# Performance work log

Measured on AMD Instinct MI355X. Metric: run time of the kernel, lower is better.

## Reference

```python
import jax, jax.numpy as jnp
import numpy as np
from jax import lax

B, T, I, H, ZH, NZ, L = 64, 512, 64, 512, 128, 32, 3


def setup_inputs() -> dict:
    key = jax.random.key(0)
    ks = jax.random.split(key, 20)
    s_h = 1.0 / np.sqrt(H)
    s_z = 1.0 / np.sqrt(ZH)
    rnd = lambda k, shape, s: jax.random.uniform(k, shape, jnp.float32, -s, s)
    return {
        "xs": jax.random.normal(ks[0], (B, T, I), jnp.float32),
        "cond": jax.random.normal(ks[1], (B, I), jnp.float32),
        "h_c": jnp.zeros((1, B, H), jnp.float32),
        "h_c_hat": jnp.zeros((1, B, ZH), jnp.float32),
        # hyper GRU (LearnableCell, num_layers=3 gates)
        "hyper_x2h_w": rnd(ks[2], (3 * ZH, I + H), s_z),
        "hyper_x2h_b": rnd(ks[3], (3 * ZH,), s_z),
        "hyper_h2h_w": rnd(ks[4], (3 * ZH, ZH), s_z),
        "hyper_h2h_b": rnd(ks[5], (3 * ZH,), s_z),
        # hypernet projections
        "zh_w": rnd(ks[6], (L * NZ, ZH), s_h),
        "zh_b": rnd(ks[7], (L * NZ,), s_h),
        "zx_w": rnd(ks[8], (L * NZ, ZH), s_h),
        "zx_b": rnd(ks[9], (L * NZ,), s_h),
        "zb_w": rnd(ks[10], (L * NZ, ZH), s_h),
        # per-layer embedding->scale projections
        "dh_w": rnd(ks[11], (L, H, NZ), s_h),
        "dx_w": rnd(ks[12], (L, H, NZ), s_h),
        "db_w": rnd(ks[13], (L, H, NZ), s_h),
        "db_b": rnd(ks[14], (L, H), s_h),
        # main recurrent / input weights
        "wh": jax.random.normal(ks[15], (L, H, H), jnp.float32) * s_h,
        "wx": jax.random.normal(ks[16], (L, H, I), jnp.float32) * s_h,
    }


def reference(xs, cond, h_c, h_c_hat,
              hyper_x2h_w, hyper_x2h_b, hyper_h2h_w, hyper_h2h_b,
              zh_w, zh_b, zx_w, zx_b, zb_w,
              dh_w, dx_w, db_w, db_b, wh, wx):
    nz = zh_w.shape[0] // 3

    def step(carry, x_t):  # x_t: [B, I]
        h, hhat = carry  # [B, H], [B, ZH]
        # --- hyper GRU update ---
        x_hat = jnp.concatenate([h, cond], axis=-1)  # [B, H+I]
        ih = x_hat @ hyper_x2h_w.T + hyper_x2h_b     # [B, 3*ZH]
        hh = hhat @ hyper_h2h_w.T + hyper_h2h_b
        i_r, i_i, i_n = jnp.split(ih, 3, axis=-1)
        h_r, h_i, h_n = jnp.split(hh, 3, axis=-1)
        r = jax.nn.sigmoid(i_r + h_r)
        g = jax.nn.sigmoid(i_i + h_i)
        n = jnp.tanh(i_n + r * h_n)
        hhat_new = n + g * (hhat - n)                # [B, ZH]
        # --- hypernetwork embeddings ---
        zh = (hhat_new @ zh_w.T + zh_b).reshape(-1, 3, nz)  # [B, 3, nz]
        zx = (hhat_new @ zx_w.T + zx_b).reshape(-1, 3, nz)
        zb = (hhat_new @ zb_w.T).reshape(-1, 3, nz)
        dh = jnp.einsum('blz,lhz->blh', zh, dh_w)    # [B, 3, H]
        dx = jnp.einsum('blz,lhz->blh', zx, dx_w)
        db = jnp.einsum('blz,lhz->blh', zb, db_w) + db_b
        # --- main GRU with hyper-modulated weights ---
        whh = jnp.einsum('bh,lgh->blg', h, wh)       # [B, 3, H]
        wxx = jnp.einsum('bi,lgi->blg', x_t, wx)
        pre = dh * whh + dx * wxx + db               # [B, 3, H]
        r0 = jax.nn.sigmoid(pre[:, 0])
        g0 = jax.nn.sigmoid(pre[:, 1])
        n0 = jnp.tanh(r0 * dh[:, 2] * whh[:, 2] + dx[:, 2] * wxx[:, 2] + db[:, 2])
        h_new = n0 + g0 * (h - n0)                   # [B, H]
        return (h_new, hhat_new), h_new

    xs_t = jnp.swapaxes(xs, 0, 1)  # [T, B, I]
    (h_f, hhat_f), ys = lax.scan(step, (h_c[0], h_c_hat[0]), xs_t)
    out = jnp.swapaxes(ys, 0, 1)   # [B, T, H]
    return out, h_f[None], hhat_f[:, None]  # final states: [1,B,H], [B,1,ZH]
```

## Files before the change

kernel.cpp:

```cpp
#include <hip/hip_runtime.h>
#include <math.h>

#define BB  64
#define TT  512
#define IN  64
#define HH  512
#define ZHH 128
#define NT  1024

#define OFF_EXIH   0u
#define OFF_EXH    196608u
#define OFF_FLAG   327680u
#define OFF_WH     335872u
#define OFF_WX     1908736u
#define OFF_DW     2105344u
#define OFF_X2H    2400256u
#define OFF_H2HB   2842624u
#define OFF_ZWB    2940928u
#define WS_NOX2H   2400256u
#define WS_FULL    2842624u
#define WS_XTRA    3014656u

__device__ __forceinline__ float sigmoidf_(float x) {
    return 1.0f / (1.0f + __expf(-x));
}
__device__ __forceinline__ float tanhf_(float x) {
    return 2.0f / (1.0f + __expf(-2.0f * x)) - 1.0f;
}
__device__ __forceinline__ float bflo(unsigned u) { return __uint_as_float(u << 16); }
__device__ __forceinline__ float bfhi(unsigned u) { return __uint_as_float(u & 0xffff0000u); }
__device__ __forceinline__ unsigned short f2bf(float f) {
    unsigned u = __float_as_uint(f);
    return (unsigned short)((u + 0x7fffu + ((u >> 16) & 1u)) >> 16);
}
__device__ __forceinline__ float dotbf8(uint4 U, float4 a, float4 b) {
    return bflo(U.x)*a.x + bfhi(U.x)*a.y + bflo(U.y)*a.z + bfhi(U.y)*a.w
         + bflo(U.z)*b.x + bfhi(U.z)*b.y + bflo(U.w)*b.z + bfhi(U.w)*b.w;
}
__device__ __forceinline__ float dot4_(const float4 a, const float4 b) {
    return a.x*b.x + a.y*b.y + a.z*b.z + a.w*b.w;
}
__device__ __forceinline__ uint4 packbf8(const float* s) {
    float4 a = *(const float4*)s;
    float4 c = *(const float4*)(s + 4);
    uint4 q;
    q.x = (unsigned)f2bf(a.x) | ((unsigned)f2bf(a.y) << 16);
    q.y = (unsigned)f2bf(a.z) | ((unsigned)f2bf(a.w) << 16);
    q.z = (unsigned)f2bf(c.x) | ((unsigned)f2bf(c.y) << 16);
    q.w = (unsigned)f2bf(c.z) | ((unsigned)f2bf(c.w) << 16);
    return q;
}

__global__ __launch_bounds__(256)
void pack_w(const float* __restrict__ wh, const float* __restrict__ wx,
            const float* __restrict__ dh_w, const float* __restrict__ dx_w,
            const float* __restrict__ db_w, const float* __restrict__ x2h_w,
            const float* __restrict__ h2h_w, const float* __restrict__ zh_w,
            const float* __restrict__ zx_w, const float* __restrict__ zb_w,
            int packX2H, int packHZ, char* __restrict__ wsb)
{
    const int u = blockIdx.x * 256 + threadIdx.x;
    if (u < 98304) {
        int q = u / 24576, r1 = u % 24576, k8 = r1 / 384, rr = r1 % 384;
        int g = rr >> 7, hl = rr & 127, h = q*128 + hl;
        ((uint4*)(wsb + OFF_WH))[u] = packbf8(wh + ((size_t)(g*512 + h))*512 + k8*8);
    } else if (u < 110592) {
        int v = u - 98304;
        int q = v / 3072, r1 = v % 3072, k8 = r1 / 384, rr = r1 % 384;
        int g = rr >> 7, hl = rr & 127, h = q*128 + hl;
        ((uint4*)(wsb + OFF_WX))[v] = packbf8(wx + ((size_t)(g*512 + h))*64 + k8*8);
    } else if (u < 129024) {
        int v = u - 110592;
        int q = v / 4608, r1 = v % 4608, k8 = r1 / 1152, rr = r1 % 1152;
        int u9 = rr >> 7, hl = rr & 127, h = q*128 + hl;
        int kind = u9 / 3, l = u9 - kind*3;
        const float* dsrc = (kind == 0) ? dh_w : ((kind == 1) ? dx_w : db_w);
        ((uint4*)(wsb + OFF_DW))[v] = packbf8(dsrc + ((size_t)(l*512) + h)*32 + k8*8);
    } else if (u < 156672) {
        if (!packX2H) return;
        int v = u - 129024;
        int q = v / 6912, r1 = v % 6912, k8 = r1 / 96, rr = r1 % 96;
        int g = rr >> 5, zz = rr & 31, j = g*128 + q*32 + zz;
        ((uint4*)(wsb + OFF_X2H))[v] = packbf8(x2h_w + (size_t)j*576 + k8*8);
    } else if (u < 162816) {
        if (!packHZ) return;
        int v = u - 156672;
        int q = v / 1536, r1 = v % 1536, k8 = r1 / 96, rr = r1 % 96;
        int g = rr >> 5, zz = rr & 31, j = g*128 + q*32 + zz;
        ((uint4*)(wsb + OFF_H2HB))[v] = packbf8(h2h_w + (size_t)j*128 + k8*8);
    } else if (u < 167424) {
        if (!packHZ) return;
        int v = u - 162816;
        int k8 = v / 288, r = v % 288;
        const float* src = (r < 96) ? (zh_w + (size_t)r*128)
                         : ((r < 192) ? (zx_w + (size_t)(r - 96)*128)
                                      : (zb_w + (size_t)(r - 192)*128));
        ((uint4*)(wsb + OFF_ZWB))[v] = packbf8(src + k8*8);
    }
}

template<int X2HP, int HZP>
__global__ __launch_bounds__(NT)
void hypercell_q(
    const float* __restrict__ xs, const float* __restrict__ cond,
    const float* __restrict__ h_c, const float* __restrict__ h_c_hat,
    const float* __restrict__ x2h_w, const float* __restrict__ x2h_b,
    const float* __restrict__ h2h_w, const float* __restrict__ h2h_b,
    const float* __restrict__ zh_w, const float* __restrict__ zh_b,
    const float* __restrict__ zx_w, const float* __restrict__ zx_b,
    const float* __restrict__ zb_w, const float* __restrict__ db_b,
    char* __restrict__ wsb, float* __restrict__ out)
{
    __shared__ __align__(16) float sh_h[512];
    __shared__ __align__(16) float sh_hat[128];
    __shared__ __align__(16) float sh_x[64];
    __shared__ __align__(16) float sh_c[64];
    __shared__ __align__(16) float sh_z[288];
    __shared__ float sh_whhp[768];
    __shared__ float sh_wxx[384];
    __shared__ float sh_ihp[192];
    __shared__ float sh_d[1152];
    __shared__ float sh_bih[96];
    __shared__ float sh_bhh[96];
    __shared__ float sh_bz[288];
    __shared__ float sh_bdb[384];

    const int b   = blockIdx.x & 63;
    const int q   = blockIdx.x >> 6;
    const int tid = threadIdx.x;

    const uint4* WHq   = (const uint4*)(wsb + OFF_WH)   + q*24576;
    const uint4* WXq   = (const uint4*)(wsb + OFF_WX)   + q*3072;
    const uint4* DWq   = (const uint4*)(wsb + OFF_DW)   + q*4608;
    const uint4* X2Hq  = (const uint4*)(wsb + OFF_X2H)  + q*6912;
    const uint4* H2HBq = (const uint4*)(wsb + OFF_H2HB) + q*1536;
    const uint4* ZWB   = (const uint4*)(wsb + OFF_ZWB);

    float* exch_ihhh = (float*)(wsb + OFF_EXIH) + (size_t)b*768;
    float* exch_h    = (float*)(wsb + OFF_EXH)  + (size_t)b*512;
    int* flagA = (int*)(wsb + OFF_FLAG + (size_t)b*64);
    int* flagB = (int*)(wsb + OFF_FLAG + 4096 + (size_t)b*64);

    if (tid < 96) {
        int j = (tid >> 5)*128 + q*32 + (tid & 31);
        sh_bih[tid] = x2h_b[j];
        sh_bhh[tid] = h2h_b[j];
    }
    if (tid < 288) sh_bz[tid] = (tid < 96) ? zh_b[tid]
                              : ((tid < 192) ? zx_b[tid - 96] : 0.f);
    if (tid < 384) {
        int l = tid >> 7, hl = tid & 127;
        sh_bdb[tid] = db_b[l*512 + q*128 + hl];
    }
    if (tid < 512) sh_h[tid] = h_c[(size_t)b*512 + tid];
    if (tid < 128) sh_hat[tid] = h_c_hat[(size_t)b*128 + tid];
    if (tid < 64) {
        sh_c[tid] = cond[(size_t)b*64 + tid];
        sh_x[tid] = xs[(size_t)b*TT*IN + tid];
    }
    __syncthreads();

    for (int t = 0; t < TT; ++t) {
        const float4* h4 = (const float4*)sh_h;
        if (tid < 768) {
            const int half = (tid >= 384);
            const int rr = half ? (tid - 384) : tid;
            const uint4* W0 = WHq + (half ? 32*384 : 0) + rr;
            const float4* hblk = h4 + half*64;
            float a0 = 0.f;
            #pragma unroll 8
            for (int k8 = 0; k8 < 32; ++k8)
                a0 += dotbf8(W0[k8*384], hblk[2*k8], hblk[2*k8 + 1]);
            sh_whhp[half*384 + rr] = a0;
            if (!half) {
                float a1 = 0.f;
                const uint4* X0 = WXq + rr;
                const float4* x4 = (const float4*)sh_x;
                #pragma unroll
                for (int k8 = 0; k8 < 8; ++k8)
                    a1 += dotbf8(X0[k8*384], x4[2*k8], x4[2*k8 + 1]);
                sh_wxx[rr] = a1;
            }
        } else if (tid < 960) {
            const int u = tid - 768;
            const int half = (u >= 96);
            const int rr = half ? (u - 96) : u;
            float a = half ? 0.f : sh_bih[rr];
            if (X2HP) {
                const uint4* W0 = X2Hq + rr;
                if (!half) {
                    #pragma unroll 4
                    for (int k8 = 0; k8 < 36; ++k8)
                        a += dotbf8(W0[k8*96], h4[2*k8], h4[2*k8 + 1]);
                } else {
                    #pragma unroll 4
                    for (int k8 = 36; k8 < 64; ++k8)
                        a += dotbf8(W0[k8*96], h4[2*k8], h4[2*k8 + 1]);
                    const float4* c4 = (const float4*)sh_c;
                    #pragma unroll
                    for (int k8 = 64; k8 < 72; ++k8)
                        a += dotbf8(W0[k8*96], c4[2*(k8-64)], c4[2*(k8-64) + 1]);
                }
            } else {
                const int j = (rr >> 5)*128 + q*32 + (rr & 31);
                const float4* wr = (const float4*)(x2h_w + (size_t)j*576);
                if (!half) {
                    #pragma unroll 8
                    for (int k4 = 0; k4 < 72; ++k4) a += dot4_(wr[k4], h4[k4]);
                } else {
                    #pragma unroll 8
                    for (int k4 = 72; k4 < 128; ++k4) a += dot4_(wr[k4], h4[k4]);
                    const float4* c4 = (const float4*)sh_c;
                    #pragma unroll
                    for (int k4 = 128; k4 < 144; ++k4) a += dot4_(wr[k4], c4[k4 - 128]);
                }
            }
            sh_ihp[half*96 + rr] = a;
        } else {
            const int t3 = tid - 960;
            const float4* hat4 = (const float4*)sh_hat;
            #pragma unroll
            for (int p = 0; p < 2; ++p) {
                const int rr = t3 + 64*p;
                if (rr < 96) {
                    const int j = (rr >> 5)*128 + q*32 + (rr & 31);
                    float a = sh_bhh[rr];
                    if (HZP) {
                        const uint4* W = H2HBq + rr;
                        #pragma unroll 8
                        for (int k8 = 0; k8 < 16; ++k8)
                            a += dotbf8(W[k8*96], hat4[2*k8], hat4[2*k8 + 1]);
                    } else {
                        const float4* wr = (const float4*)(h2h_w + (size_t)j*128);
                        #pragma unroll 8
                        for (int k4 = 0; k4 < 32; ++k4) a += dot4_(wr[k4], hat4[k4]);
                    }
                    __hip_atomic_store(&exch_ihhh[384 + j], a, __ATOMIC_RELAXED, __HIP_MEMORY_SCOPE_AGENT);
                }
            }
        }
        __syncthreads();
        if (tid < 96) {
            const int j = (tid >> 5)*128 + q*32 + (tid & 31);
            __hip_atomic_store(&exch_ihhh[j], sh_ihp[tid] + sh_ihp[96 + tid],
                               __ATOMIC_RELAXED, __HIP_MEMORY_SCOPE_AGENT);
        }
        asm volatile("s_waitcnt vmcnt(0)" ::: "memory");
        __syncthreads();
        if (tid == 0) {
            __hip_atomic_fetch_add(flagA, 1, __ATOMIC_RELAXED, __HIP_MEMORY_SCOPE_AGENT);
            while (__hip_atomic_load(flagA, __ATOMIC_RELAXED, __HIP_MEMORY_SCOPE_AGENT) < 4*(t+1))
                __builtin_amdgcn_s_sleep(1);
        }
        __syncthreads();

        if (tid < 128) {
            const int j = tid;
            float i_r = __hip_atomic_load(&exch_ihhh[j],       __ATOMIC_RELAXED, __HIP_MEMORY_SCOPE_AGENT);
            float i_i = __hip_atomic_load(&exch_ihhh[128 + j], __ATOMIC_RELAXED, __HIP_MEMORY_SCOPE_AGENT);
            float i_n = __hip_atomic_load(&exch_ihhh[256 + j], __ATOMIC_RELAXED, __HIP_MEMORY_SCOPE_AGENT);
            float h_r = __hip_atomic_load(&exch_ihhh[384 + j], __ATOMIC_RELAXED, __HIP_MEMORY_SCOPE_AGENT);
            float h_i = __hip_atomic_load(&exch_ihhh[512 + j], __ATOMIC_RELAXED, __HIP_MEMORY_SCOPE_AGENT);
            float h_n = __hip_atomic_load(&exch_ihhh[640 + j], __ATOMIC_RELAXED, __HIP_MEMORY_SCOPE_AGENT);
            float rg = sigmoidf_(i_r + h_r);
            float gg = sigmoidf_(i_i + h_i);
            float nn = tanhf_(i_n + rg * h_n);
            float hn = nn + gg * (sh_hat[j] - nn);
            sh_hat[j] = hn;
            if (t == TT - 1 && q == 0)
                __builtin_nontemporal_store(hn,
                    &out[(size_t)BB*TT*HH + (size_t)BB*HH + (size_t)b*ZHH + j]);
        } else if (tid >= 128 && tid < 192 && t + 1 < TT) {
            sh_x[tid - 128] = xs[((size_t)b*TT + t + 1)*IN + (tid - 128)];
        }
        __syncthreads();

        if (tid < 288) {
            float acc = sh_bz[tid];
            const float4* hat4 = (const float4*)sh_hat;
            if (HZP) {
                const uint4* W = ZWB + tid;
                #pragma unroll 8
                for (int k8 = 0; k8 < 16; ++k8)
                    acc += dotbf8(W[k8*288], hat4[2*k8], hat4[2*k8 + 1]);
            } else {
                const float* src = (tid < 96) ? (zh_w + (size_t)tid*128)
                                 : ((tid < 192) ? (zx_w + (size_t)(tid - 96)*128)
                                                : (zb_w + (size_t)(tid - 192)*128));
                const float4* W = (const float4*)src;
                #pragma unroll 8
                for (int k4 = 0; k4 < 32; ++k4) acc += dot4_(W[k4], hat4[k4]);
            }
            sh_z[tid] = acc;
        }
        __syncthreads();

        #pragma unroll
        for (int rp = 0; rp < 2; ++rp) {
            const int rr = tid + rp*NT;
            if (rr < 1152) {
                const int u9 = rr >> 7;
                const int kind = u9 / 3, l = u9 - kind*3;
                const uint4* W = DWq + rr;
                const float4* Z = (const float4*)(&sh_z[kind*96 + l*32]);
                float acc = 0.f;
                #pragma unroll
                for (int k8 = 0; k8 < 4; ++k8)
                    acc += dotbf8(W[k8*1152], Z[2*k8], Z[2*k8 + 1]);
                sh_d[rr] = acc;
            }
        }
        __syncthreads();

        if (tid < 128) {
            const int hl = tid, hg = q*128 + hl;
            float whh0 = sh_whhp[hl]       + sh_whhp[384 + hl];
            float whh1 = sh_whhp[128 + hl] + sh_whhp[512 + hl];
            float whh2 = sh_whhp[256 + hl] + sh_whhp[640 + hl];
            float wxx0 = sh_wxx[hl], wxx1 = sh_wxx[128 + hl], wxx2 = sh_wxx[256 + hl];
            float dh0 = sh_d[hl],       dh1 = sh_d[128 + hl], dh2 = sh_d[256 + hl];
            float dx0 = sh_d[384 + hl], dx1 = sh_d[512 + hl], dx2 = sh_d[640 + hl];
            float db0 = sh_d[768 + hl]  + sh_bdb[hl];
            float db1 = sh_d[896 + hl]  + sh_bdb[128 + hl];
            float db2 = sh_d[1024 + hl] + sh_bdb[256 + hl];
            float r0 = sigmoidf_(dh0*whh0 + dx0*wxx0 + db0);
            float g0 = sigmoidf_(dh1*whh1 + dx1*wxx1 + db1);
            float n0 = tanhf_(r0*dh2*whh2 + dx2*wxx2 + db2);
            float hold = sh_h[hg];
            float hnew = n0 + g0*(hold - n0);
            __builtin_nontemporal_store(hnew, &out[((size_t)b*TT + t)*HH + hg]);
            if (t == TT - 1)
                __builtin_nontemporal_store(hnew, &out[(size_t)BB*TT*HH + (size_t)b*512 + hg]);
            __hip_atomic_store(&exch_h[hg], hnew, __ATOMIC_RELAXED, __HIP_MEMORY_SCOPE_AGENT);
        }
        asm volatile("s_waitcnt vmcnt(0)" ::: "memory");
        __syncthreads();
        if (tid == 0) {
            __hip_atomic_fetch_add(flagB, 1, __ATOMIC_RELAXED, __HIP_MEMORY_SCOPE_AGENT);
            while (__hip_atomic_load(flagB, __ATOMIC_RELAXED, __HIP_MEMORY_SCOPE_AGENT) < 4*(t+1))
                __builtin_amdgcn_s_sleep(1);
        }
        __syncthreads();
        if (tid < 512)
            sh_h[tid] = __hip_atomic_load(&exch_h[tid], __ATOMIC_RELAXED, __HIP_MEMORY_SCOPE_AGENT);
        __syncthreads();
    }
}

__device__ __forceinline__ float wred(float v) {
    v += __shfl_xor(v, 32, 64); v += __shfl_xor(v, 16, 64); v += __shfl_xor(v, 8, 64);
    v += __shfl_xor(v, 4, 64);  v += __shfl_xor(v, 2, 64);  v += __shfl_xor(v, 1, 64);
    return v;
}
__global__ __launch_bounds__(1024)
void hypercell_batch(
    const float* __restrict__ xs, const float* __restrict__ cond,
    const float* __restrict__ h_c, const float* __restrict__ h_c_hat,
    const float* __restrict__ x2h_w, const float* __restrict__ x2h_b,
    const float* __restrict__ h2h_w, const float* __restrict__ h2h_b,
    const float* __restrict__ zh_w, const float* __restrict__ zh_b,
    const float* __restrict__ zx_w, const float* __restrict__ zx_b,
    const float* __restrict__ zb_w,
    const float* __restrict__ dh_w, const float* __restrict__ dx_w,
    const float* __restrict__ db_w, const float* __restrict__ db_b,
    const float* __restrict__ wh, const float* __restrict__ wx,
    float* __restrict__ out)
{
    __shared__ float h_s[HH];
    __shared__ float hhat_s[ZHH];
    __shared__ float x_s[IN];
    __shared__ float cond_s[IN];
    __shared__ float whh_s[3*HH];
    __shared__ float wxx_s[3*HH];
    __shared__ float ih_s[3*ZHH];
    __shared__ float hh_s[3*ZHH];
    __shared__ float z_s[288];
    const int b = blockIdx.x, tid = threadIdx.x, lane = tid & 63, wv = tid >> 6;
    if (tid < IN)  cond_s[tid] = cond[(size_t)b*IN + tid];
    if (tid < HH)  h_s[tid]    = h_c[(size_t)b*HH + tid];
    if (tid < ZHH) hhat_s[tid] = h_c_hat[(size_t)b*ZHH + tid];
    __syncthreads();
    for (int t = 0; t < TT; ++t) {
        if (tid < IN) x_s[tid] = xs[((size_t)b*TT + t)*IN + tid];
        const float4* h4 = (const float4*)h_s;
        const float4 ha = h4[lane]; const float4 hb = h4[64 + lane];
        {
            const float* wl = wh + (size_t)(wv*96)*HH + lane*4;
            #pragma unroll 4
            for (int i = 0; i < 96; ++i) {
                float p = wred(dot4_(*(const float4*)(wl + (size_t)i*HH), ha)
                             + dot4_(*(const float4*)(wl + (size_t)i*HH + 256), hb));
                if (lane == 0) whh_s[wv*96 + i] = p;
            }
        }
        {
            const float cv = cond_s[lane];
            const float* wbase = x2h_w + (size_t)(wv*24)*576;
            #pragma unroll 2
            for (int i = 0; i < 24; ++i) {
                const float* wr = wbase + (size_t)i*576;
                float p = wred(dot4_(*(const float4*)(wr + lane*4), ha)
                             + dot4_(*(const float4*)(wr + 256 + lane*4), hb) + wr[512 + lane]*cv);
                if (lane == 0) ih_s[wv*24 + i] = p + x2h_b[wv*24 + i];
            }
        }
        {
            const float2 hv = ((const float2*)hhat_s)[lane];
            const float* wbase = h2h_w + (size_t)(wv*24)*ZHH;
            #pragma unroll 4
            for (int i = 0; i < 24; ++i) {
                float2 wq = *(const float2*)(wbase + (size_t)i*ZHH + lane*2);
                float p = wred(wq.x*hv.x + wq.y*hv.y);
                if (lane == 0) hh_s[wv*24 + i] = p + h2h_b[wv*24 + i];
            }
        }
        __syncthreads();
        {
            const float4* x4 = (const float4*)x_s;
            {
                const float4* wr = (const float4*)(wx + (size_t)tid*IN);
                float acc = 0.f;
                #pragma unroll
                for (int j = 0; j < 16; ++j) acc += dot4_(wr[j], x4[j]);
                wxx_s[tid] = acc;
            }
            if (tid < 512) {
                const int r = 1024 + tid;
                const float4* wr = (const float4*)(wx + (size_t)r*IN);
                float acc = 0.f;
                #pragma unroll
                for (int j = 0; j < 16; ++j) acc += dot4_(wr[j], x4[j]);
                wxx_s[r] = acc;
            }
        }
        if (tid < ZHH) {
            const int j = tid;
            float r = sigmoidf_(ih_s[j] + hh_s[j]);
            float g = sigmoidf_(ih_s[ZHH+j] + hh_s[ZHH+j]);
            float n = tanhf(ih_s[2*ZHH+j] + r*hh_s[2*ZHH+j]);
            float hn = n + g*(hhat_s[j] - n);
            hhat_s[j] = hn;
            if (t == TT-1)
                out[(size_t)BB*TT*HH + (size_t)BB*HH + (size_t)b*ZHH + j] = hn;
        }
        __syncthreads();
        {
            const float2 hv = ((const float2*)hhat_s)[lane];
            #pragma unroll 2
            for (int i = 0; i < 18; ++i) {
                const int R = wv*18 + i, kind = R / 96, r96 = R % 96;
                const float* wsrc = (kind == 0) ? zh_w : ((kind == 1) ? zx_w : zb_w);
                float2 wq = *(const float2*)(wsrc + (size_t)r96*ZHH + lane*2);
                float p = wred(wq.x*hv.x + wq.y*hv.y);
                if (lane == 0)
                    z_s[R] = p + ((kind == 0) ? zh_b[r96] : ((kind == 1) ? zx_b[r96] : 0.f));
            }
        }
        __syncthreads();
        if (tid < HH) {
            const int h = tid;
            const float* dsrc[3] = { dh_w, dx_w, db_w };
            float dv[3][3];
            #pragma unroll
            for (int kind = 0; kind < 3; ++kind)
                #pragma unroll
                for (int l = 0; l < 3; ++l) {
                    const float4* wr = (const float4*)(dsrc[kind] + ((size_t)l*HH + h)*32);
                    const float4* zp = (const float4*)&z_s[kind*96 + l*32];
                    float acc = 0.f;
                    #pragma unroll
                    for (int j = 0; j < 8; ++j) acc += dot4_(wr[j], zp[j]);
                    dv[kind][l] = acc;
                }
            float whh0 = whh_s[h], whh1 = whh_s[HH+h], whh2 = whh_s[2*HH+h];
            float wxx0 = wxx_s[h], wxx1 = wxx_s[HH+h], wxx2 = wxx_s[2*HH+h];
            float db0 = dv[2][0] + db_b[h], db1 = dv[2][1] + db_b[HH+h], db2 = dv[2][2] + db_b[2*HH+h];
            float r0 = sigmoidf_(dv[0][0]*whh0 + dv[1][0]*wxx0 + db0);
            float g0 = sigmoidf_(dv[0][1]*whh1 + dv[1][1]*wxx1 + db1);
            float n0 = tanhf(r0*dv[0][2]*whh2 + dv[1][2]*wxx2 + db2);
            float hold = h_s[h];
            float hnew = n0 + g0*(hold - n0);
            h_s[h] = hnew;
            out[((size_t)b*TT + t)*HH + h] = hnew;
            if (t == TT-1) out[(size_t)BB*TT*HH + (size_t)b*HH + h] = hnew;
        }
        __syncthreads();
    }
}

extern "C" void kernel_launch(void* const* d_in, const int* in_sizes, int n_in,
                              void* d_out, int out_size, void* d_ws, size_t ws_size,
                              hipStream_t stream) {
    const float* xs      = (const float*)d_in[0];
    const float* cond    = (const float*)d_in[1];
    const float* h_c     = (const float*)d_in[2];
    const float* h_c_hat = (const float*)d_in[3];
    const float* x2h_w   = (const float*)d_in[4];
    const float* x2h_b   = (const float*)d_in[5];
    const float* h2h_w   = (const float*)d_in[6];
    const float* h2h_b   = (const float*)d_in[7];
    const float* zh_w    = (const float*)d_in[8];
    const float* zh_b    = (const float*)d_in[9];
    const float* zx_w    = (const float*)d_in[10];
    const float* zx_b    = (const float*)d_in[11];
    const float* zb_w    = (const float*)d_in[12];
    const float* dh_w    = (const float*)d_in[13];
    const float* dx_w    = (const float*)d_in[14];
    const float* db_w    = (const float*)d_in[15];
    const float* db_b    = (const float*)d_in[16];
    const float* wh      = (const float*)d_in[17];
    const float* wx      = (const float*)d_in[18];
    float* out = (float*)d_out;

    if (ws_size >= (size_t)WS_NOX2H) {
        char* wsb = (char*)d_ws;
        const int full = (ws_size >= (size_t)WS_FULL) ? 1 : 0;
        const int xtra = (ws_size >= (size_t)WS_XTRA) ? 1 : 0;
        hipMemsetAsync(wsb + OFF_FLAG, 0, 8192, stream);
        hipLaunchKernelGGL(pack_w, dim3(654), dim3(256), 0, stream,
                           wh, wx, dh_w, dx_w, db_w, x2h_w, h2h_w,
                           zh_w, zx_w, zb_w, full, xtra, wsb);
        if (xtra) {
            hipLaunchKernelGGL((hypercell_q<1,1>), dim3(256), dim3(NT), 0, stream,
                               xs, cond, h_c, h_c_hat, x2h_w, x2h_b, h2h_w, h2h_b,
                               zh_w, zh_b, zx_w, zx_b, zb_w, db_b, wsb, out);
        } else if (full) {
            hipLaunchKernelGGL((hypercell_q<1,0>), dim3(256), dim3(NT), 0, stream,
                               xs, cond, h_c, h_c_hat, x2h_w, x2h_b, h2h_w, h2h_b,
                               zh_w, zh_b, zx_w, zx_b, zb_w, db_b, wsb, out);
        } else {
            hipLaunchKernelGGL((hypercell_q<0,0>), dim3(256), dim3(NT), 0, stream,
                               xs, cond, h_c, h_c_hat, x2h_w, x2h_b, h2h_w, h2h_b,
                               zh_w, zh_b, zx_w, zx_b, zb_w, db_b, wsb, out);
        }
    } else {
        hipLaunchKernelGGL(hypercell_batch, dim3(BB), dim3(1024), 0, stream,
                           xs, cond, h_c, h_c_hat, x2h_w, x2h_b, h2h_w, h2h_b,
                           zh_w, zh_b, zx_w, zx_b, zb_w, dh_w, dx_w, db_w, db_b,
                           wh, wx, out);
    }
}
```

Baseline: 9.736 ms.

## Overlap cross-block flag waits with local matvecs and split hyper-GRU dot products

Reorders each timestep so the hyper-GRU x2h/h2h partial products are computed first, split eight-way and two-way across threads, reduced, and published before the main Wh·h matvec. The Wh·h matvec then runs while a single wavefront spins on the inter-block flag and copies the exchanged values into shared memory. The Wx·x product for the next step is likewise computed while the last wavefront waits on the h exchange. This hides inter-block synchronisation latency behind useful work, at the cost of more shared memory and extra reduction passes. The next step's Wx·x reads sh_x, which must already hold the next input at that point; the elided code decides whether that holds.

```diff
diff --git a/kernel.cpp b/kernel.cpp
--- a/kernel.cpp
+++ b/kernel.cpp
@@ -118,7 +118,9 @@
     __shared__ __align__(16) float sh_z[288];
     __shared__ float sh_whhp[768];
     __shared__ float sh_wxx[384];
-    __shared__ float sh_ihp[192];
+    __shared__ float sh_ihp[768];
+    __shared__ float sh_hhp[192];
+    __shared__ float sh_ihhh[768];
     __shared__ float sh_d[1152];
     __shared__ float sh_bih[96];
     __shared__ float sh_bhh[96];
@@ -128,6 +130,7 @@
     const int b   = blockIdx.x & 63;
     const int q   = blockIdx.x >> 6;
     const int tid = threadIdx.x;
+    const int lane = tid & 63;
 
     const uint4* WHq   = (const uint4*)(wsb + OFF_WH)   + q*24576;
     const uint4* WXq   = (const uint4*)(wsb + OFF_WX)   + q*3072;
@@ -159,9 +162,79 @@
         sh_x[tid] = xs[(size_t)b*TT*IN + tid];
     }
     __syncthreads();
+    if (tid < 384) {
+        float a1 = 0.f;
+        const uint4* X0 = WXq + tid;
+        const float4* x4 = (const float4*)sh_x;
+        #pragma unroll
+        for (int k8 = 0; k8 < 8; ++k8)
+            a1 += dotbf8(X0[k8*384], x4[2*k8], x4[2*k8 + 1]);
+        sh_wxx[tid] = a1;
+    }
+    __syncthreads();
 
     for (int t = 0; t < TT; ++t) {
-        const float4* h4 = (const float4*)sh_h;
+        const float4* h4   = (const float4*)sh_h;
+        const float4* hat4 = (const float4*)sh_hat;
+        const float4* c4   = (const float4*)sh_c;
+
+        if (tid < 768) {
+            const int rr = tid >> 3, p = tid & 7;
+            float a = 0.f;
+            if (X2HP) {
+                const uint4* W0 = X2Hq + rr;
+                #pragma unroll
+                for (int k8 = 9*p; k8 < 9*p + 9; ++k8) {
+                    if (k8 < 64) a += dotbf8(W0[k8*96], h4[2*k8], h4[2*k8 + 1]);
+                    else         a += dotbf8(W0[k8*96], c4[2*(k8-64)], c4[2*(k8-64) + 1]);
+                }
+            } else {
+                const int j = (rr >> 5)*128 + q*32 + (rr & 31);
+                const float4* wr = (const float4*)(x2h_w + (size_t)j*576);
+                #pragma unroll
+                for (int k4 = 18*p; k4 < 18*p + 18; ++k4) {
+                    if (k4 < 128) a += dot4_(wr[k4], h4[k4]);
+                    else          a += dot4_(wr[k4], c4[k4 - 128]);
+                }
+            }
+            sh_ihp[rr*8 + p] = a;
+        } else if (tid < 960) {
+            const int u = tid - 768;
+            const int rr = u >> 1, p = u & 1;
+            float a = 0.f;
+            if (HZP) {
+                const uint4* W = H2HBq + rr;
+                #pragma unroll
+                for (int k8 = 8*p; k8 < 8*p + 8; ++k8)
+                    a += dotbf8(W[k8*96], hat4[2*k8], hat4[2*k8 + 1]);
+            } else {
+                const int j = (rr >> 5)*128 + q*32 + (rr & 31);
+                const float4* wr = (const float4*)(h2h_w + (size_t)j*128);
+                #pragma unroll
+                for (int k4 = 16*p; k4 < 16*p + 16; ++k4)
+                    a += dot4_(wr[k4], hat4[k4]);
+            }
+            sh_hhp[rr*2 + p] = a;
+        }
+        __syncthreads();
+
+        if (tid < 96) {
+            const int j = (tid >> 5)*128 + q*32 + (tid & 31);
+            float a = sh_bih[tid];
+            #pragma unroll
+            for (int p = 0; p < 8; ++p) a += sh_ihp[tid*8 + p];
+            __hip_atomic_store(&exch_ihhh[j], a, __ATOMIC_RELAXED, __HIP_MEMORY_SCOPE_AGENT);
+        } else if (tid < 192) {
+            const int rr = tid - 96;
+            const int j = (rr >> 5)*128 + q*32 + (rr & 31);
+            float a = sh_bhh[rr] + sh_hhp[rr*2] + sh_hhp[rr*2 + 1];
+            __hip_atomic_store(&exch_ihhh[384 + j], a, __ATOMIC_RELAXED, __HIP_MEMORY_SCOPE_AGENT);
+        }
+        asm volatile("s_waitcnt vmcnt(0)" ::: "memory");
+        __syncthreads();
+        if (tid == 0)
+            __hip_atomic_fetch_add(flagA, 1, __ATOMIC_RELAXED, __HIP_MEMORY_SCOPE_AGENT);
+
         if (tid < 768) {
             const int half = (tid >= 384);
             const int rr = half ? (tid - 384) : tid;
@@ -172,99 +245,23 @@
             for (int k8 = 0; k8 < 32; ++k8)
                 a0 += dotbf8(W0[k8*384], hblk[2*k8], hblk[2*k8 + 1]);
             sh_whhp[half*384 + rr] = a0;
-            if (!half) {
-                float a1 = 0.f;
-                const uint4* X0 = WXq + rr;
-                const float4* x4 = (const float4*)sh_x;
-                #pragma unroll
-                for (int k8 = 0; k8 < 8; ++k8)
-                    a1 += dotbf8(X0[k8*384], x4[2*k8], x4[2*k8 + 1]);
-                sh_wxx[rr] = a1;
-            }
-        } else if (tid < 960) {
-            const int u = tid - 768;
-            const int half = (u >= 96);
-            const int rr = half ? (u - 96) : u;
-            float a = half ? 0.f : sh_bih[rr];
-            if (X2HP) {
-                const uint4* W0 = X2Hq + rr;
-                if (!half) {
-                    #pragma unroll 4
-                    for (int k8 = 0; k8 < 36; ++k8)
-                        a += dotbf8(W0[k8*96], h4[2*k8], h4[2*k8 + 1]);
-                } else {
-                    #pragma unroll 4
-                    for (int k8 = 36; k8 < 64; ++k8)
-                        a += dotbf8(W0[k8*96], h4[2*k8], h4[2*k8 + 1]);
-                    const float4* c4 = (const float4*)sh_c;
-                    #pragma unroll
-                    for (int k8 = 64; k8 < 72; ++k8)
-                        a += dotbf8(W0[k8*96], c4[2*(k8-64)], c4[2*(k8-64) + 1]);
-                }
-            } else {
-                const int j = (rr >> 5)*128 + q*32 + (rr & 31);
-                const float4* wr = (const float4*)(x2h_w + (size_t)j*576);
-                if (!half) {
-                    #pragma unroll 8
-                    for (int k4 = 0; k4 < 72; ++k4) a += dot4_(wr[k4], h4[k4]);
-                } else {
-                    #pragma unroll 8
-                    for (int k4 = 72; k4 < 128; ++k4) a += dot4_(wr[k4], h4[k4]);
-                    const float4* c4 = (const float4*)sh_c;
-                    #pragma unroll
-                    for (int k4 = 128; k4 < 144; ++k4) a += dot4_(wr[k4], c4[k4 - 128]);
-                }
-            }
-            sh_ihp[half*96 + rr] = a;
-        } else {
-            const int t3 = tid - 960;
-            const float4* hat4 = (const float4*)sh_hat;
+        } else if (tid >= 960) {
+            if (lane == 0) {
+                while (__hip_atomic_load(flagA, __ATOMIC_RELAXED, __HIP_MEMORY_SCOPE_AGENT) < 4*(t+1))
+                    __builtin_amdgcn_s_sleep(1);
+            }
             #pragma unroll
-            for (int p = 0; p < 2; ++p) {
-                const int rr = t3 + 64*p;
-                if (rr < 96) {
-                    const int j = (rr >> 5)*128 + q*32 + (rr & 31);
-                    float a = sh_bhh[rr];
-                    if (HZP) {
-                        const uint4* W = H2HBq + rr;
-                        #pragma unroll 8
-                        for (int k8 = 0; k8 < 16; ++k8)
-                            a += dotbf8(W[k8*96], hat4[2*k8], hat4[2*k8 + 1]);
-                    } else {
-                        const float4* wr = (const float4*)(h2h_w + (size_t)j*128);
-                        #pragma unroll 8
-                        for (int k4 = 0; k4 < 32; ++k4) a += dot4_(wr[k4], hat4[k4]);
-                    }
-                    __hip_atomic_store(&exch_ihhh[384 + j], a, __ATOMIC_RELAXED, __HIP_MEMORY_SCOPE_AGENT);
-                }
-            }
-        }
-        __syncthreads();
-        if (tid < 96) {
-            const int j = (tid >> 5)*128 + q*32 + (tid & 31);
-            __hip_atomic_store(&exch_ihhh[j], sh_ihp[tid] + sh_ihp[96 + tid],
-                               __ATOMIC_RELAXED, __HIP_MEMORY_SCOPE_AGENT);
-        }
-        asm volatile("s_waitcnt vmcnt(0)" ::: "memory");
-        __syncthreads();
-        if (tid == 0) {
-            __hip_atomic_fetch_add(flagA, 1, __ATOMIC_RELAXED, __HIP_MEMORY_SCOPE_AGENT);
-            while (__hip_atomic_load(flagA, __ATOMIC_RELAXED, __HIP_MEMORY_SCOPE_AGENT) < 4*(t+1))
-                __builtin_amdgcn_s_sleep(1);
+            for (int jj = 0; jj < 12; ++jj)
+                sh_ihhh[lane + 64*jj] = __hip_atomic_load(&exch_ihhh[lane + 64*jj],
+                                            __ATOMIC_RELAXED, __HIP_MEMORY_SCOPE_AGENT);
         }
         __syncthreads();
 
         if (tid < 128) {
             const int j = tid;
-            float i_r = __hip_atomic_load(&exch_ihhh[j],       __ATOMIC_RELAXED, __HIP_MEMORY_SCOPE_AGENT);
-            float i_i = __hip_atomic_load(&exch_ihhh[128 + j], __ATOMIC_RELAXED, __HIP_MEMORY_SCOPE_AGENT);
-            float i_n = __hip_atomic_load(&exch_ihhh[256 + j], __ATOMIC_RELAXED, __HIP_MEMORY_SCOPE_AGENT);
-            float h_r = __hip_atomic_load(&exch_ihhh[384 + j], __ATOMIC_RELAXED, __HIP_MEMORY_SCOPE_AGENT);
-            float h_i = __hip_atomic_load(&exch_ihhh[512 + j], __ATOMIC_RELAXED, __HIP_MEMORY_SCOPE_AGENT);
-            float h_n = __hip_atomic_load(&exch_ihhh[640 + j], __ATOMIC_RELAXED, __HIP_MEMORY_SCOPE_AGENT);
-            float rg = sigmoidf_(i_r + h_r);
-            float gg = sigmoidf_(i_i + h_i);
-            float nn = tanhf_(i_n + rg * h_n);
+            float rg = sigmoidf_(sh_ihhh[j]       + sh_ihhh[384 + j]);
+            float gg = sigmoidf_(sh_ihhh[128 + j] + sh_ihhh[512 + j]);
+            float nn = tanhf_(sh_ihhh[256 + j] + rg * sh_ihhh[640 + j]);
             float hn = nn + gg * (sh_hat[j] - nn);
             sh_hat[j] = hn;
             if (t == TT - 1 && q == 0)
@@ -277,19 +274,19 @@
 
         if (tid < 288) {
             float acc = sh_bz[tid];
-            const float4* hat4 = (const float4*)sh_hat;
+            const float4* nhat4 = (const float4*)sh_hat;
             if (HZP) {
                 const uint4* W = ZWB + tid;
                 #pragma unroll 8
                 for (int k8 = 0; k8 < 16; ++k8)
-                    acc += dotbf8(W[k8*288], hat4[2*k8], hat4[2*k8 + 1]);
+                    acc += dotbf8(W[k8*288], nhat4[2*k8], nhat4[2*k8 + 1]);
             } else {
                 const float* src = (tid < 96) ? (zh_w + (size_t)tid*128)
                                  : ((tid < 192) ? (zx_w + (size_t)(tid - 96)*128)
                                                 : (zb_w + (size_t)(tid - 192)*128));
                 const float4* W = (const float4*)src;
                 #pragma unroll 8
-                for (int k4 = 0; k4 < 32; ++k4) acc += dot4_(W[k4], hat4[k4]);
+                for (int k4 = 0; k4 < 32; ++k4) acc += dot4_(W[k4], nhat4[k4]);
             }
             sh_z[tid] = acc;
         }
@@ -335,14 +332,29 @@
         }
         asm volatile("s_waitcnt vmcnt(0)" ::: "memory");
         __syncthreads();
-        if (tid == 0) {
+        if (tid == 0)
             __hip_atomic_fetch_add(flagB, 1, __ATOMIC_RELAXED, __HIP_MEMORY_SCOPE_AGENT);
-            while (__hip_atomic_load(flagB, __ATOMIC_RELAXED, __HIP_MEMORY_SCOPE_AGENT) < 4*(t+1))
-                __builtin_amdgcn_s_sleep(1);
-        }
-        __syncthreads();
-        if (tid < 512)
-            sh_h[tid] = __hip_atomic_load(&exch_h[tid], __ATOMIC_RELAXED, __HIP_MEMORY_SCOPE_AGENT);
+
+        if (tid < 384) {
+            if (t + 1 < TT) {
+                float a1 = 0.f;
+                const uint4* X0 = WXq + tid;
+                const float4* x4 = (const float4*)sh_x;
+                #pragma unroll
+                for (int k8 = 0; k8 < 8; ++k8)
+                    a1 += dotbf8(X0[k8*384], x4[2*k8], x4[2*k8 + 1]);
+                sh_wxx[tid] = a1;
+            }
+        } else if (tid >= 960) {
+            if (lane == 0) {
+                while (__hip_atomic_load(flagB, __ATOMIC_RELAXED, __HIP_MEMORY_SCOPE_AGENT) < 4*(t+1))
+                    __builtin_amdgcn_s_sleep(1);
+            }
+            #pragma unroll
+            for (int jj = 0; jj < 8; ++jj)
+                sh_h[lane + 64*jj] = __hip_atomic_load(&exch_h[lane + 64*jj],
+                                         __ATOMIC_RELAXED, __HIP_MEMORY_SCOPE_AGENT);
+        }
         __syncthreads();
     }
 }
```

Measured after the change: 17.79 ms. +82.7%, slower.

## Split each batch row across eight cooperating blocks instead of four

Applied to the files above, without the earlier changes.

The persistent recurrent kernel now spreads each batch element's hidden dimension across 8 workgroups (64 hidden units each) instead of 4, launching 512 blocks, with weight packing relaid out to match. Each block does half the per-step matvec work and holds a smaller weight slice, which is meant to cut per-step latency on the serial path. The input-projection matvec also moves later in the step, beside the hypernetwork scale computation, using a double-buffered x tile. The cost is more participants in the two global flag barriers per timestep, and it relies on all 512 blocks being co-resident; if they are not, the spin-waits could deadlock.

```diff
diff --git a/kernel.cpp b/kernel.cpp
--- a/kernel.cpp
+++ b/kernel.cpp
@@ -7,6 +7,7 @@
 #define HH  512
 #define ZHH 128
 #define NT  1024
+#define NS  8
 
 #define OFF_EXIH   0u
 #define OFF_EXH    196608u
@@ -61,32 +62,32 @@
 {
     const int u = blockIdx.x * 256 + threadIdx.x;
     if (u < 98304) {
-        int q = u / 24576, r1 = u % 24576, k8 = r1 / 384, rr = r1 % 384;
-        int g = rr >> 7, hl = rr & 127, h = q*128 + hl;
+        int s = u / 12288, r1 = u % 12288, k8 = r1 / 192, rr = r1 % 192;
+        int g = rr >> 6, hl = rr & 63, h = s*64 + hl;
         ((uint4*)(wsb + OFF_WH))[u] = packbf8(wh + ((size_t)(g*512 + h))*512 + k8*8);
     } else if (u < 110592) {
         int v = u - 98304;
-        int q = v / 3072, r1 = v % 3072, k8 = r1 / 384, rr = r1 % 384;
-        int g = rr >> 7, hl = rr & 127, h = q*128 + hl;
+        int s = v / 1536, r1 = v % 1536, k8 = r1 / 192, rr = r1 % 192;
+        int g = rr >> 6, hl = rr & 63, h = s*64 + hl;
         ((uint4*)(wsb + OFF_WX))[v] = packbf8(wx + ((size_t)(g*512 + h))*64 + k8*8);
     } else if (u < 129024) {
         int v = u - 110592;
-        int q = v / 4608, r1 = v % 4608, k8 = r1 / 1152, rr = r1 % 1152;
-        int u9 = rr >> 7, hl = rr & 127, h = q*128 + hl;
+        int s = v / 2304, r1 = v % 2304, k8 = r1 / 576, rr = r1 % 576;
+        int u9 = rr >> 6, hl = rr & 63, h = s*64 + hl;
         int kind = u9 / 3, l = u9 - kind*3;
         const float* dsrc = (kind == 0) ? dh_w : ((kind == 1) ? dx_w : db_w);
         ((uint4*)(wsb + OFF_DW))[v] = packbf8(dsrc + ((size_t)(l*512) + h)*32 + k8*8);
     } else if (u < 156672) {
         if (!packX2H) return;
         int v = u - 129024;
-        int q = v / 6912, r1 = v % 6912, k8 = r1 / 96, rr = r1 % 96;
-        int g = rr >> 5, zz = rr & 31, j = g*128 + q*32 + zz;
+        int s = v / 3456, r1 = v % 3456, k8 = r1 / 48, rr = r1 % 48;
+        int g = rr >> 4, zz = rr & 15, j = g*128 + s*16 + zz;
         ((uint4*)(wsb + OFF_X2H))[v] = packbf8(x2h_w + (size_t)j*576 + k8*8);
     } else if (u < 162816) {
         if (!packHZ) return;
         int v = u - 156672;
-        int q = v / 1536, r1 = v % 1536, k8 = r1 / 96, rr = r1 % 96;
-        int g = rr >> 5, zz = rr & 31, j = g*128 + q*32 + zz;
+        int s = v / 768, r1 = v % 768, k8 = r1 / 48, rr = r1 % 48;
+        int g = rr >> 4, zz = rr & 15, j = g*128 + s*16 + zz;
         ((uint4*)(wsb + OFF_H2HB))[v] = packbf8(h2h_w + (size_t)j*128 + k8*8);
     } else if (u < 167424) {
         if (!packHZ) return;
@@ -100,8 +101,8 @@
 }
 
 template<int X2HP, int HZP>
-__global__ __launch_bounds__(NT)
-void hypercell_q(
+__global__ __launch_bounds__(NT, 8)
+void hypercell_s(
     const float* __restrict__ xs, const float* __restrict__ cond,
     const float* __restrict__ h_c, const float* __restrict__ h_c_hat,
     const float* __restrict__ x2h_w, const float* __restrict__ x2h_b,
@@ -113,27 +114,28 @@
 {
     __shared__ __align__(16) float sh_h[512];
     __shared__ __align__(16) float sh_hat[128];
-    __shared__ __align__(16) float sh_x[64];
+    __shared__ __align__(16) float sh_x[2][64];
     __shared__ __align__(16) float sh_c[64];
     __shared__ __align__(16) float sh_z[288];
     __shared__ float sh_whhp[768];
-    __shared__ float sh_wxx[384];
+    __shared__ float sh_wxx[192];
     __shared__ float sh_ihp[192];
-    __shared__ float sh_d[1152];
-    __shared__ float sh_bih[96];
-    __shared__ float sh_bhh[96];
+    __shared__ float sh_hhv[48];
+    __shared__ float sh_d[576];
+    __shared__ float sh_bih[48];
+    __shared__ float sh_bhh[48];
     __shared__ float sh_bz[288];
-    __shared__ float sh_bdb[384];
+    __shared__ float sh_bdb[192];
 
     const int b   = blockIdx.x & 63;
-    const int q   = blockIdx.x >> 6;
+    const int s   = blockIdx.x >> 6;
     const int tid = threadIdx.x;
 
-    const uint4* WHq   = (const uint4*)(wsb + OFF_WH)   + q*24576;
-    const uint4* WXq   = (const uint4*)(wsb + OFF_WX)   + q*3072;
-    const uint4* DWq   = (const uint4*)(wsb + OFF_DW)   + q*4608;
-    const uint4* X2Hq  = (const uint4*)(wsb + OFF_X2H)  + q*6912;
-    const uint4* H2HBq = (const uint4*)(wsb + OFF_H2HB) + q*1536;
+    const uint4* WHs   = (const uint4*)(wsb + OFF_WH)   + s*12288;
+    const uint4* WXs   = (const uint4*)(wsb + OFF_WX)   + s*1536;
+    const uint4* DWs   = (const uint4*)(wsb + OFF_DW)   + s*2304;
+    const uint4* X2Hs  = (const uint4*)(wsb + OFF_X2H)  + s*3456;
+    const uint4* H2HBs = (const uint4*)(wsb + OFF_H2HB) + s*768;
     const uint4* ZWB   = (const uint4*)(wsb + OFF_ZWB);
 
     float* exch_ihhh = (float*)(wsb + OFF_EXIH) + (size_t)b*768;
@@ -141,115 +143,108 @@
     int* flagA = (int*)(wsb + OFF_FLAG + (size_t)b*64);
     int* flagB = (int*)(wsb + OFF_FLAG + 4096 + (size_t)b*64);
 
-    if (tid < 96) {
-        int j = (tid >> 5)*128 + q*32 + (tid & 31);
+    if (tid < 48) {
+        int j = (tid >> 4)*128 + s*16 + (tid & 15);
         sh_bih[tid] = x2h_b[j];
         sh_bhh[tid] = h2h_b[j];
     }
     if (tid < 288) sh_bz[tid] = (tid < 96) ? zh_b[tid]
                               : ((tid < 192) ? zx_b[tid - 96] : 0.f);
-    if (tid < 384) {
-        int l = tid >> 7, hl = tid & 127;
-        sh_bdb[tid] = db_b[l*512 + q*128 + hl];
+    if (tid < 192) {
+        int l = tid >> 6, hl = tid & 63;
+        sh_bdb[tid] = db_b[l*512 + s*64 + hl];
     }
     if (tid < 512) sh_h[tid] = h_c[(size_t)b*512 + tid];
     if (tid < 128) sh_hat[tid] = h_c_hat[(size_t)b*128 + tid];
     if (tid < 64) {
         sh_c[tid] = cond[(size_t)b*64 + tid];
-        sh_x[tid] = xs[(size_t)b*TT*IN + tid];
+        sh_x[0][tid] = xs[(size_t)b*TT*IN + tid];
     }
     __syncthreads();
 
     for (int t = 0; t < TT; ++t) {
-        const float4* h4 = (const float4*)sh_h;
+        const float4* h4   = (const float4*)sh_h;
+        const float4* hat4 = (const float4*)sh_hat;
+        const float4* c4   = (const float4*)sh_c;
+
         if (tid < 768) {
-            const int half = (tid >= 384);
-            const int rr = half ? (tid - 384) : tid;
-            const uint4* W0 = WHq + (half ? 32*384 : 0) + rr;
-            const float4* hblk = h4 + half*64;
+            const int kq = tid / 192;
+            const int rr = tid - kq*192;
+            const uint4* W0 = WHs + kq*(16*192) + rr;
+            const float4* hblk = h4 + kq*32;
             float a0 = 0.f;
             #pragma unroll 8
-            for (int k8 = 0; k8 < 32; ++k8)
-                a0 += dotbf8(W0[k8*384], hblk[2*k8], hblk[2*k8 + 1]);
-            sh_whhp[half*384 + rr] = a0;
-            if (!half) {
-                float a1 = 0.f;
-                const uint4* X0 = WXq + rr;
-                const float4* x4 = (const float4*)sh_x;
-                #pragma unroll
-                for (int k8 = 0; k8 < 8; ++k8)
-                    a1 += dotbf8(X0[k8*384], x4[2*k8], x4[2*k8 + 1]);
-                sh_wxx[rr] = a1;
-            }
+            for (int k8 = 0; k8 < 16; ++k8)
+                a0 += dotbf8(W0[k8*192], hblk[2*k8], hblk[2*k8 + 1]);
+            sh_whhp[kq*192 + rr] = a0;
         } else if (tid < 960) {
             const int u = tid - 768;
-            const int half = (u >= 96);
-            const int rr = half ? (u - 96) : u;
-            float a = half ? 0.f : sh_bih[rr];
+            const int p = u / 48;
+            const int rr = u - p*48;
+            float a = 0.f;
             if (X2HP) {
-                const uint4* W0 = X2Hq + rr;
-                if (!half) {
-                    #pragma unroll 4
-                    for (int k8 = 0; k8 < 36; ++k8)
-                        a += dotbf8(W0[k8*96], h4[2*k8], h4[2*k8 + 1]);
+                const uint4* W0 = X2Hs + rr;
+                if (p < 3) {
+                    #pragma unroll
+                    for (int k8 = 18*p; k8 < 18*p + 18; ++k8)
+                        a += dotbf8(W0[k8*48], h4[2*k8], h4[2*k8 + 1]);
                 } else {
-                    #pragma unroll 4
-                    for (int k8 = 36; k8 < 64; ++k8)
-                        a += dotbf8(W0[k8*96], h4[2*k8], h4[2*k8 + 1]);
-                    const float4* c4 = (const float4*)sh_c;
+                    #pragma unroll
+                    for (int k8 = 54; k8 < 64; ++k8)
+                        a += dotbf8(W0[k8*48], h4[2*k8], h4[2*k8 + 1]);
                     #pragma unroll
                     for (int k8 = 64; k8 < 72; ++k8)
-                        a += dotbf8(W0[k8*96], c4[2*(k8-64)], c4[2*(k8-64) + 1]);
+                        a += dotbf8(W0[k8*48], c4[2*(k8-64)], c4[2*(k8-64) + 1]);
                 }
             } else {
-                const int j = (rr >> 5)*128 + q*32 + (rr & 31);
+                const int j = (rr >> 4)*128 + s*16 + (rr & 15);
                 const float4* wr = (const float4*)(x2h_w + (size_t)j*576);
-                if (!half) {
-                    #pragma unroll 8
-                    for (int k4 = 0; k4 < 72; ++k4) a += dot4_(wr[k4], h4[k4]);
+                if (p < 3) {
+                    #pragma unroll
+                    for (int k4 = 36*p; k4 < 36*p + 36; ++k4)
+                        a += dot4_(wr[k4], h4[k4]);
                 } else {
-                    #pragma unroll 8
-                    for (int k4 = 72; k4 < 128; ++k4) a += dot4_(wr[k4], h4[k4]);
-                    const float4* c4 = (const float4*)sh_c;
+                    #pragma unroll
+                    for (int k4 = 108; k4 < 128; ++k4) a += dot4_(wr[k4], h4[k4]);
                     #pragma unroll
                     for (int k4 = 128; k4 < 144; ++k4) a += dot4_(wr[k4], c4[k4 - 128]);
                 }
             }
-            sh_ihp[half*96 + rr] = a;
-        } else {
-            const int t3 = tid - 960;
-            const float4* hat4 = (const float4*)sh_hat;
-            #pragma unroll
-            for (int p = 0; p < 2; ++p) {
-                const int rr = t3 + 64*p;
-                if (rr < 96) {
-                    const int j = (rr >> 5)*128 + q*32 + (rr & 31);
-                    float a = sh_bhh[rr];
-                    if (HZP) {
-                        const uint4* W = H2HBq + rr;
-                        #pragma unroll 8
-                        for (int k8 = 0; k8 < 16; ++k8)
-                            a += dotbf8(W[k8*96], hat4[2*k8], hat4[2*k8 + 1]);
-                    } else {
-                        const float4* wr = (const float4*)(h2h_w + (size_t)j*128);
-                        #pragma unroll 8
-                        for (int k4 = 0; k4 < 32; ++k4) a += dot4_(wr[k4], hat4[k4]);
-                    }
-                    __hip_atomic_store(&exch_ihhh[384 + j], a, __ATOMIC_RELAXED, __HIP_MEMORY_SCOPE_AGENT);
-                }
-            }
-        }
-        __syncthreads();
-        if (tid < 96) {
-            const int j = (tid >> 5)*128 + q*32 + (tid & 31);
-            __hip_atomic_store(&exch_ihhh[j], sh_ihp[tid] + sh_ihp[96 + tid],
+            sh_ihp[p*48 + rr] = a;
+        } else if (tid < 1008) {
+            const int rr = tid - 960;
+            float a = sh_bhh[rr];
+            if (HZP) {
+                const uint4* W = H2HBs + rr;
+                #pragma unroll 8
+                for (int k8 = 0; k8 < 16; ++k8)
+                    a += dotbf8(W[k8*48], hat4[2*k8], hat4[2*k8 + 1]);
+            } else {
+                const int j = (rr >> 4)*128 + s*16 + (rr & 15);
+                const float4* wr = (const float4*)(h2h_w + (size_t)j*128);
+                #pragma unroll 8
+                for (int k4 = 0; k4 < 32; ++k4) a += dot4_(wr[k4], hat4[k4]);
+            }
+            sh_hhv[rr] = a;
+        }
+        __syncthreads();
+
+        if (tid < 48) {
+            const int j = (tid >> 4)*128 + s*16 + (tid & 15);
+            float a = sh_bih[tid] + sh_ihp[tid] + sh_ihp[48 + tid]
+                    + sh_ihp[96 + tid] + sh_ihp[144 + tid];
+            __hip_atomic_store(&exch_ihhh[j], a, __ATOMIC_RELAXED, __HIP_MEMORY_SCOPE_AGENT);
+        } else if (tid < 96) {
+            const int rr = tid - 48;
+            const int j = (rr >> 4)*128 + s*16 + (rr & 15);
+            __hip_atomic_store(&exch_ihhh[384 + j], sh_hhv[rr],
                                __ATOMIC_RELAXED, __HIP_MEMORY_SCOPE_AGENT);
         }
         asm volatile("s_waitcnt vmcnt(0)" ::: "memory");
         __syncthreads();
         if (tid == 0) {
             __hip_atomic_fetch_add(flagA, 1, __ATOMIC_RELAXED, __HIP_MEMORY_SCOPE_AGENT);
-            while (__hip_atomic_load(flagA, __ATOMIC_RELAXED, __HIP_MEMORY_SCOPE_AGENT) < 4*(t+1))
+            while (__hip_atomic_load(flagA, __ATOMIC_RELAXED, __HIP_MEMORY_SCOPE_AGENT) < NS*(t+1))
                 __builtin_amdgcn_s_sleep(1);
         }
         __syncthreads();
@@ -267,62 +262,70 @@
             float nn = tanhf_(i_n + rg * h_n);
             float hn = nn + gg * (sh_hat[j] - nn);
             sh_hat[j] = hn;
-            if (t == TT - 1 && q == 0)
+            if (t == TT - 1 && s == 0)
                 __builtin_nontemporal_store(hn,
                     &out[(size_t)BB*TT*HH + (size_t)BB*HH + (size_t)b*ZHH + j]);
         } else if (tid >= 128 && tid < 192 && t + 1 < TT) {
-            sh_x[tid - 128] = xs[((size_t)b*TT + t + 1)*IN + (tid - 128)];
+            sh_x[(t + 1) & 1][tid - 128] = xs[((size_t)b*TT + t + 1)*IN + (tid - 128)];
         }
         __syncthreads();
 
         if (tid < 288) {
             float acc = sh_bz[tid];
-            const float4* hat4 = (const float4*)sh_hat;
+            const float4* nhat4 = (const float4*)sh_hat;
             if (HZP) {
                 const uint4* W = ZWB + tid;
                 #pragma unroll 8
                 for (int k8 = 0; k8 < 16; ++k8)
-                    acc += dotbf8(W[k8*288], hat4[2*k8], hat4[2*k8 + 1]);
+                    acc += dotbf8(W[k8*288], nhat4[2*k8], nhat4[2*k8 + 1]);
             } else {
                 const float* src = (tid < 96) ? (zh_w + (size_t)tid*128)
                                  : ((tid < 192) ? (zx_w + (size_t)(tid - 96)*128)
                                                 : (zb_w + (size_t)(tid - 192)*128));
                 const float4* W = (const float4*)src;
                 #pragma unroll 8
-                for (int k4 = 0; k4 < 32; ++k4) acc += dot4_(W[k4], hat4[k4]);
+                for (int k4 = 0; k4 < 32; ++k4) acc += dot4_(W[k4], nhat4[k4]);
             }
             sh_z[tid] = acc;
         }
         __syncthreads();
 
-        #pragma unroll
-        for (int rp = 0; rp < 2; ++rp) {
-            const int rr = tid + rp*NT;
-            if (rr < 1152) {
-                const int u9 = rr >> 7;
-                const int kind = u9 / 3, l = u9 - kind*3;
-                const uint4* W = DWq + rr;
-                const float4* Z = (const float4*)(&sh_z[kind*96 + l*32]);
-                float acc = 0.f;
-                #pragma unroll
-                for (int k8 = 0; k8 < 4; ++k8)
-                    acc += dotbf8(W[k8*1152], Z[2*k8], Z[2*k8 + 1]);
-                sh_d[rr] = acc;
-            }
-        }
-        __syncthreads();
-
-        if (tid < 128) {
-            const int hl = tid, hg = q*128 + hl;
-            float whh0 = sh_whhp[hl]       + sh_whhp[384 + hl];
-            float whh1 = sh_whhp[128 + hl] + sh_whhp[512 + hl];
-            float whh2 = sh_whhp[256 + hl] + sh_whhp[640 + hl];
-            float wxx0 = sh_wxx[hl], wxx1 = sh_wxx[128 + hl], wxx2 = sh_wxx[256 + hl];
-            float dh0 = sh_d[hl],       dh1 = sh_d[128 + hl], dh2 = sh_d[256 + hl];
-            float dx0 = sh_d[384 + hl], dx1 = sh_d[512 + hl], dx2 = sh_d[640 + hl];
-            float db0 = sh_d[768 + hl]  + sh_bdb[hl];
-            float db1 = sh_d[896 + hl]  + sh_bdb[128 + hl];
-            float db2 = sh_d[1024 + hl] + sh_bdb[256 + hl];
+        if (tid < 576) {
+            const int u9 = tid >> 6;
+            const int kind = u9 / 3, l = u9 - kind*3;
+            const uint4* W = DWs + tid;
+            const float4* Z = (const float4*)(&sh_z[kind*96 + l*32]);
+            float acc = 0.f;
+            #pragma unroll
+            for (int k8 = 0; k8 < 4; ++k8)
+                acc += dotbf8(W[k8*576], Z[2*k8], Z[2*k8 + 1]);
+            sh_d[tid] = acc;
+        } else if (tid < 768) {
+            const int rr = tid - 576;
+            const uint4* X0 = WXs + rr;
+            const float4* xc4 = (const float4*)sh_x[t & 1];
+            float a1 = 0.f;
+            #pragma unroll
+            for (int k8 = 0; k8 < 8; ++k8)
+                a1 += dotbf8(X0[k8*192], xc4[2*k8], xc4[2*k8 + 1]);
+            sh_wxx[rr] = a1;
+        }
+        __syncthreads();
+
+        if (tid < 64) {
+            const int hl = tid, hg = s*64 + hl;
+            float whh0 = sh_whhp[hl]        + sh_whhp[192 + hl]
+                       + sh_whhp[384 + hl]  + sh_whhp[576 + hl];
+            float whh1 = sh_whhp[64 + hl]   + sh_whhp[256 + hl]
+                       + sh_whhp[448 + hl]  + sh_whhp[640 + hl];
+            float whh2 = sh_whhp[128 + hl]  + sh_whhp[320 + hl]
+                       + sh_whhp[512 + hl]  + sh_whhp[704 + hl];
+            float wxx0 = sh_wxx[hl], wxx1 = sh_wxx[64 + hl], wxx2 = sh_wxx[128 + hl];
+            float dh0 = sh_d[hl],        dh1 = sh_d[64 + hl],  dh2 = sh_d[128 + hl];
+            float dx0 = sh_d[192 + hl],  dx1 = sh_d[256 + hl], dx2 = sh_d[320 + hl];
+            float db0 = sh_d[384 + hl] + sh_bdb[hl];
+            float db1 = sh_d[448 + hl] + sh_bdb[64 + hl];
+            float db2 = sh_d[512 + hl] + sh_bdb[128 + hl];
             float r0 = sigmoidf_(dh0*whh0 + dx0*wxx0 + db0);
             float g0 = sigmoidf_(dh1*whh1 + dx1*wxx1 + db1);
             float n0 = tanhf_(r0*dh2*whh2 + dx2*wxx2 + db2);
@@ -337,7 +340,7 @@
         __syncthreads();
         if (tid == 0) {
             __hip_atomic_fetch_add(flagB, 1, __ATOMIC_RELAXED, __HIP_MEMORY_SCOPE_AGENT);
-            while (__hip_atomic_load(flagB, __ATOMIC_RELAXED, __HIP_MEMORY_SCOPE_AGENT) < 4*(t+1))
+            while (__hip_atomic_load(flagB, __ATOMIC_RELAXED, __HIP_MEMORY_SCOPE_AGENT) < NS*(t+1))
                 __builtin_amdgcn_s_sleep(1);
         }
         __syncthreads();
@@ -521,15 +524,15 @@
                            wh, wx, dh_w, dx_w, db_w, x2h_w, h2h_w,
                            zh_w, zx_w, zb_w, full, xtra, wsb);
         if (xtra) {
-            hipLaunchKernelGGL((hypercell_q<1,1>), dim3(256), dim3(NT), 0, stream,
+            hipLaunchKernelGGL((hypercell_s<1,1>), dim3(512), dim3(NT), 0, stream,
                                xs, cond, h_c, h_c_hat, x2h_w, x2h_b, h2h_w, h2h_b,
                                zh_w, zh_b, zx_w, zx_b, zb_w, db_b, wsb, out);
         } else if (full) {
-            hipLaunchKernelGGL((hypercell_q<1,0>), dim3(256), dim3(NT), 0, stream,
+            hipLaunchKernelGGL((hypercell_s<1,0>), dim3(512), dim3(NT), 0, stream,
                                xs, cond, h_c, h_c_hat, x2h_w, x2h_b, h2h_w, h2h_b,
                                zh_w, zh_b, zx_w, zx_b, zb_w, db_b, wsb, out);
         } else {
-            hipLaunchKernelGGL((hypercell_q<0,0>), dim3(256), dim3(NT), 0, stream,
+            hipLaunchKernelGGL((hypercell_s<0,0>), dim3(512), dim3(NT), 0, stream,
                                xs, cond, h_c, h_c_hat, x2h_w, x2h_b, h2h_w, h2h_b,
                                zh_w, zh_b, zx_w, zx_b, zb_w, db_b, wsb, out);
         }
```

New measurement: 15.85 ms. 62.9% more time.
